# Optimization experiments

Hardware: AMD Instinct MI355X
Metric: run time of the kernel (lower is better)

The kernel has to match this reference:

```python
import jax, jax.numpy as jnp
import numpy as np

B, S, HID = 2, 2048, 2048
H, KVH, D = 16, 8, 128           # query heads, kv heads, head_dim
G = H // KVH                      # num_key_value_groups
EPS = 1e-6
SCALE = D ** -0.5
ROPE_THETA = 1e6


def _rope_tables():
    inv_freq = 1.0 / (ROPE_THETA ** (jnp.arange(0, D, 2, dtype=jnp.float32) / D))
    freqs = jnp.arange(S, dtype=jnp.float32)[:, None] * inv_freq[None, :]   # [S, D/2]
    emb = jnp.concatenate([freqs, freqs], axis=-1)                          # [S, D]
    cos = jnp.broadcast_to(jnp.cos(emb)[None], (B, S, D))
    sin = jnp.broadcast_to(jnp.sin(emb)[None], (B, S, D))
    return cos, sin


def setup_inputs() -> dict:
    key = jax.random.key(0)
    ks = jax.random.split(key, 6)
    hidden_states = jax.random.normal(ks[0], (B, S, HID), jnp.float32)
    cos, sin = _rope_tables()
    w = 0.02
    Wq = jax.random.normal(ks[1], (HID, H * D * 2), jnp.float32) * w  # gated: q + gate
    Wk = jax.random.normal(ks[2], (HID, KVH * D), jnp.float32) * w
    Wv = jax.random.normal(ks[3], (HID, KVH * D), jnp.float32) * w
    Wo = jax.random.normal(ks[4], (H * D, HID), jnp.float32) * w
    q_norm_w = jnp.ones((D,), jnp.float32)
    k_norm_w = jnp.ones((D,), jnp.float32)
    return {"hidden_states": hidden_states, "cos": cos, "sin": sin,
            "Wq": Wq, "Wk": Wk, "Wv": Wv, "Wo": Wo,
            "q_norm_w": q_norm_w, "k_norm_w": k_norm_w}


def _rms_norm(x, w):
    # per-head RMSNorm over last dim (head_dim), computed in fp32
    var = jnp.mean(jnp.square(x.astype(jnp.float32)), axis=-1, keepdims=True)
    return (x * jax.lax.rsqrt(var + EPS)) * w


def _rotate_half(x):
    x1, x2 = x[..., : D // 2], x[..., D // 2:]
    return jnp.concatenate([-x2, x1], axis=-1)


def reference(hidden_states, cos, sin, Wq, Wk, Wv, Wo, q_norm_w, k_norm_w):
    # q_proj with output gate
    mixed_q = hidden_states @ Wq                         # [B,S,H*2D]
    mixed_q = mixed_q.reshape(B, S, H, 2 * D)
    q, gate = mixed_q[..., :D], mixed_q[..., D:]          # [B,S,H,D] each
    gate = gate.reshape(B, S, H * D)
    k = (hidden_states @ Wk).reshape(B, S, KVH, D)
    v = (hidden_states @ Wv).reshape(B, S, KVH, D)

    # per-head QK RMSNorm, then to [B, heads, S, D]
    q = _rms_norm(q, q_norm_w).transpose(0, 2, 1, 3)      # [B,H,S,D]
    k = _rms_norm(k, k_norm_w).transpose(0, 2, 1, 3)      # [B,KVH,S,D]
    v = v.transpose(0, 2, 1, 3)                           # [B,KVH,S,D]

    # RoPE (cos/sin broadcast over head dim)
    c, s = cos[:, None], sin[:, None]                     # [B,1,S,D]
    q = q * c + _rotate_half(q) * s
    k = k * c + _rotate_half(k) * s

    # GQA causal attention without materializing repeated K/V
    qg = q.reshape(B, KVH, G, S, D)
    scores = jnp.einsum('bkgqd,bkld->bkgql', qg, k) * SCALE   # [B,KVH,G,S,S]
    causal = jnp.tril(jnp.ones((S, S), dtype=bool))
    scores = jnp.where(causal, scores, jnp.finfo(scores.dtype).min)
    probs = jax.nn.softmax(scores, axis=-1)
    out = jnp.einsum('bkgql,bkld->bkgqd', probs, v)           # [B,KVH,G,S,D]
    out = out.reshape(B, H, S, D).transpose(0, 2, 1, 3).reshape(B, S, H * D)

    # sigmoid-gated output, then o_proj
    out = out * jax.nn.sigmoid(gate)
    return out @ Wo
```

## Files before the change

kernel.cpp:

```cpp
#include <hip/hip_runtime.h>
#include <hip/hip_bf16.h>

#define B_ 2
#define S_ 2048
#define HID_ 2048
#define H_ 16
#define KVH_ 8
#define D_ 128
#define G_ 2
#define EPS_ 1e-6f
#define SCALE_ 0.08838834764831845f
#define SCALE2_ 0.1275313760443445f
#define NQKV 6144

typedef __hip_bfloat16 bf16;
typedef __attribute__((ext_vector_type(8))) short s8v;
typedef __attribute__((ext_vector_type(4))) float f4v;

__device__ __forceinline__ unsigned short f2b(float f) {
    __hip_bfloat16 h = __float2bfloat16(f);
    return *reinterpret_cast<unsigned short*>(&h);
}
__device__ __forceinline__ float b2f(short u) {
    unsigned int x = ((unsigned int)(unsigned short)u) << 16;
    return __builtin_bit_cast(float, x);
}

__device__ __forceinline__ f4v MFMA(s8v a, s8v b, f4v c) {
    return __builtin_amdgcn_mfma_f32_16x16x32_bf16(a, b, c, 0, 0, 0);
}

__device__ __forceinline__ void gl_lds16(const void* g, void* l) {
    __builtin_amdgcn_global_load_lds(
        (const __attribute__((address_space(1))) void*)g,
        (__attribute__((address_space(3))) void*)l, 16, 0, 0);
}

__device__ __forceinline__ void cstore(float* p, float v) { *p = v; }
__device__ __forceinline__ void cstore(short* p, float v) { *p = (short)f2b(v); }

template <int CTRL>
__device__ __forceinline__ float dpp_f(float x) {
    return __builtin_bit_cast(float,
        __builtin_amdgcn_update_dpp(0, __builtin_bit_cast(int, x), CTRL, 0xF, 0xF, true));
}
__device__ __forceinline__ float red16_max(float v) {
    v = fmaxf(v, dpp_f<0xB1>(v));
    v = fmaxf(v, dpp_f<0x4E>(v));
    v = fmaxf(v, dpp_f<0x124>(v));
    v = fmaxf(v, dpp_f<0x128>(v));
    return v;
}
__device__ __forceinline__ float red16_sum(float v) {
    v += dpp_f<0xB1>(v);
    v += dpp_f<0x4E>(v);
    v += dpp_f<0x124>(v);
    v += dpp_f<0x128>(v);
    return v;
}

__global__ __launch_bounds__(256) void f2bf_kernel(const float* __restrict__ in,
                                                   short* __restrict__ out, int n4) {
    int i = blockIdx.x * 256 + threadIdx.x;
    if (i >= n4) return;
    const float4 v = *(const float4*)(in + (size_t)i * 4);
    ushort4 o;
    o.x = f2b(v.x); o.y = f2b(v.y); o.z = f2b(v.z); o.w = f2b(v.w);
    *(ushort4*)(out + (size_t)i * 4) = o;
}

__global__ __launch_bounds__(256) void transpose_conv(const float* __restrict__ in,
                                                      short* __restrict__ out,
                                                      int K, int N) {
    __shared__ short t[32][33];
    const int n0 = blockIdx.x * 32, k0 = blockIdx.y * 32;
    const int tx = threadIdx.x, ty = threadIdx.y;
#pragma unroll
    for (int j = 0; j < 4; j++) {
        const int r = ty + j * 8;
        t[r][tx] = (short)f2b(in[(size_t)(k0 + r) * N + n0 + tx]);
    }
    __syncthreads();
#pragma unroll
    for (int j = 0; j < 4; j++) {
        const int r = ty + j * 8;
        out[(size_t)(n0 + r) * K + k0 + tx] = t[tx][r];
    }
}

__global__ __launch_bounds__(256) void transpose_v(const short* __restrict__ in,
                                                   short* __restrict__ out) {
    __shared__ short t[32][33];
    const int s0 = blockIdx.x * 32, d0 = blockIdx.y * 32, bk = blockIdx.z;
    const int b = bk / KVH_, kvh = bk % KVH_;
    const short* ip = in + (size_t)b * S_ * NQKV + kvh * D_;
    const int tx = threadIdx.x, ty = threadIdx.y;
#pragma unroll
    for (int j = 0; j < 4; j++) {
        const int r = ty + j * 8;
        t[r][tx] = ip[(size_t)(s0 + r) * NQKV + d0 + tx];
    }
    __syncthreads();
#pragma unroll
    for (int j = 0; j < 4; j++) {
        const int r = ty + j * 8;
        out[((size_t)bk * D_ + d0 + r) * S_ + s0 + tx] = t[tx][r];
    }
}

__global__ __launch_bounds__(512, 2) void gemm256(const short* __restrict__ A,
                                                  const short* __restrict__ Bt,
                                                  short* __restrict__ C,
                                                  int M, int N, int K) {
    __shared__ __align__(16) short As[3][256][32];
    __shared__ __align__(16) short Bs[3][256][32];
    const int tid = threadIdx.x;
    const int w = tid >> 6, l = tid & 63;
    const int lr = l & 15, g = l >> 4;
    const int nwg = gridDim.x * gridDim.y;
    int bid = blockIdx.y * gridDim.x + blockIdx.x;
    bid = (bid & 7) * (nwg >> 3) + (bid >> 3);
    const int bx = bid % gridDim.x, by = bid / gridDim.x;
    const int row0 = by * 256, col0 = bx * 256;
    const int wr = w >> 2, wc = w & 3;

    f4v acc[8][4];
#pragma unroll
    for (int i = 0; i < 8; i++)
#pragma unroll
        for (int j = 0; j < 4; j++) acc[i][j] = (f4v)0.f;

    const int srow = l >> 2;
    const int schunk = (l & 3) ^ ((l >> 3) & 3);
    const int rdslot = (g ^ ((lr >> 1) & 3)) * 8;

    auto stageA = [&](int buf, int t) {
        const int kt = t * 32;
#pragma unroll
        for (int i = 0; i < 2; i++) {
            const int rb = w * 32 + i * 16;
            gl_lds16(A + (size_t)(row0 + rb + srow) * K + kt + schunk * 8,
                     &As[buf][rb][0]);
        }
    };
    auto stageB = [&](int buf, int t) {
        const int kt = t * 32;
#pragma unroll
        for (int i = 0; i < 2; i++) {
            const int rb = w * 32 + i * 16;
            gl_lds16(Bt + (size_t)(col0 + rb + srow) * K + kt + schunk * 8,
                     &Bs[buf][rb][0]);
        }
    };

    const int nt = K >> 5;
    stageA(0, 0); stageB(0, 0);
    stageA(1, 1); stageB(1, 1);

#pragma unroll 1
    for (int t = 0; t < nt; t++) {
        const int buf = t % 3;
        const int nbuf = (t + 2) % 3;

        __builtin_amdgcn_sched_barrier(0);
        if (t + 1 < nt) {
            asm volatile("s_waitcnt vmcnt(4)" ::: "memory");
        } else {
            asm volatile("s_waitcnt vmcnt(0)" ::: "memory");
        }
        __builtin_amdgcn_sched_barrier(0);
        __builtin_amdgcn_s_barrier();
        __builtin_amdgcn_sched_barrier(0);

        s8v b[4], a[4];
#pragma unroll
        for (int ni = 0; ni < 4; ni++)
            b[ni] = *(const s8v*)&Bs[buf][wc * 64 + ni * 16 + lr][rdslot];
#pragma unroll
        for (int mi = 0; mi < 4; mi++)
            a[mi] = *(const s8v*)&As[buf][wr * 128 + mi * 16 + lr][rdslot];
        if (t + 2 < nt) stageA(nbuf, t + 2);
        __builtin_amdgcn_s_setprio(1);
#pragma unroll
        for (int mi = 0; mi < 4; mi++)
#pragma unroll
            for (int ni = 0; ni < 4; ni++)
                acc[mi][ni] = MFMA(a[mi], b[ni], acc[mi][ni]);
        __builtin_amdgcn_s_setprio(0);
        __builtin_amdgcn_s_barrier();
        __builtin_amdgcn_sched_barrier(0);

        s8v a2[4];
#pragma unroll
        for (int mi = 0; mi < 4; mi++)
            a2[mi] = *(const s8v*)&As[buf][wr * 128 + (4 + mi) * 16 + lr][rdslot];
        if (t + 2 < nt) stageB(nbuf, t + 2);
        __builtin_amdgcn_s_setprio(1);
#pragma unroll
        for (int mi = 0; mi < 4; mi++)
#pragma unroll
            for (int ni = 0; ni < 4; ni++)
                acc[4 + mi][ni] = MFMA(a2[mi], b[ni], acc[4 + mi][ni]);
        __builtin_amdgcn_s_setprio(0);
    }

#pragma unroll
    for (int mi = 0; mi < 8; mi++)
#pragma unroll
        for (int ni = 0; ni < 4; ni++) {
            const int row = row0 + wr * 128 + mi * 16 + g * 4;
            const int col = col0 + wc * 64 + ni * 16 + lr;
#pragma unroll
            for (int j = 0; j < 4; j++)
                cstore(&C[(size_t)(row + j) * N + col], acc[mi][ni][j]);
        }
}

template <typename CT, int GATED>
__global__ __launch_bounds__(256) void gemm_bt(const short* __restrict__ A,
                                               const short* __restrict__ Bt,
                                               CT* __restrict__ C,
                                               int M, int N, int K) {
    __shared__ __align__(16) short As[2][128][32];
    __shared__ __align__(16) short Bs[2][128][32];
    const int tid = threadIdx.x;
    const int w = tid >> 6, l = tid & 63;
    const int lr = l & 15, g = l >> 4;
    const int nwg = gridDim.x * gridDim.y;
    int bid = blockIdx.y * gridDim.x + blockIdx.x;
    bid = (bid & 7) * (nwg >> 3) + (bid >> 3);
    const int bx = bid % gridDim.x, by = bid / gridDim.x;
    const int row0 = by * 128, col0 = bx * 128;
    const int wr = w >> 1, wc = w & 1;

    f4v acc[4][4];
#pragma unroll
    for (int i = 0; i < 4; i++)
#pragma unroll
        for (int j = 0; j < 4; j++) acc[i][j] = (f4v)0.f;

    const int srow = l >> 2;
    const int sg = (l & 3) ^ ((srow >> 1) & 3);

    auto stage = [&](int buf, int kt) {
        const int k = kt + sg * 8;
#pragma unroll
        for (int i = 0; i < 2; i++) {
            const int rb = (w * 2 + i) * 16;
            size_t aoff;
            if constexpr (GATED)
                aoff = (size_t)(row0 + rb + srow) * NQKV + ((k >> 7) << 8) + (k & 127);
            else
                aoff = (size_t)(row0 + rb + srow) * K + k;
            gl_lds16(A + aoff, &As[buf][rb][0]);
            gl_lds16(Bt + (size_t)(col0 + rb + srow) * K + k, &Bs[buf][rb][0]);
        }
    };

    const int nt = K >> 5;
    stage(0, 0);
    stage(1, 32);
    const int rdslot = (g ^ ((lr >> 1) & 3)) * 8;

#pragma unroll 1
    for (int t = 0; t < nt; t++) {
        const int cur = t & 1;
        if (t + 1 < nt) {
            asm volatile("s_waitcnt vmcnt(4)" ::: "memory");
        } else {
            asm volatile("s_waitcnt vmcnt(0)" ::: "memory");
        }
        __builtin_amdgcn_s_barrier();
        __builtin_amdgcn_sched_barrier(0);

        s8v a[4], b[4];
#pragma unroll
        for (int mi = 0; mi < 4; mi++)
            a[mi] = *(const s8v*)&As[cur][wr * 64 + mi * 16 + lr][rdslot];
#pragma unroll
        for (int ni = 0; ni < 4; ni++)
            b[ni] = *(const s8v*)&Bs[cur][wc * 64 + ni * 16 + lr][rdslot];

        asm volatile("s_waitcnt lgkmcnt(0)" ::: "memory");
        __builtin_amdgcn_sched_barrier(0);
        __builtin_amdgcn_s_barrier();
        __builtin_amdgcn_sched_barrier(0);

        if (t + 2 < nt) stage(cur, (t + 2) * 32);

#pragma unroll
        for (int mi = 0; mi < 4; mi++)
#pragma unroll
            for (int ni = 0; ni < 4; ni++)
                acc[mi][ni] = MFMA(a[mi], b[ni], acc[mi][ni]);
    }

#pragma unroll
    for (int mi = 0; mi < 4; mi++)
#pragma unroll
        for (int ni = 0; ni < 4; ni++) {
            const int row = row0 + wr * 64 + mi * 16 + g * 4;
            const int col = col0 + wc * 64 + ni * 16 + lr;
#pragma unroll
            for (int j = 0; j < 4; j++)
                cstore(&C[(size_t)(row + j) * N + col], acc[mi][ni][j]);
        }
}

__global__ __launch_bounds__(128) void norm_rope(const bf16* __restrict__ src,
                                                 const float* __restrict__ normw,
                                                 const float* __restrict__ cosb,
                                                 const float* __restrict__ sinb,
                                                 bf16* __restrict__ dst,
                                                 int NH, int rowStride, int chanStride) {
    const int idx = blockIdx.x;
    const int h = idx % NH;
    const int s = (idx / NH) % S_;
    const int b = idx / (NH * S_);
    const int d = threadIdx.x;

    const size_t src_i = (size_t)(b * S_ + s) * rowStride + h * chanStride + d;
    const size_t dst_i = (((size_t)b * NH + h) * S_ + s) * D_ + d;

    float x = __bfloat162float(src[src_i]);
    float sq = x * x;
#pragma unroll
    for (int o = 32; o > 0; o >>= 1) sq += __shfl_down(sq, o);
    __shared__ float red[2];
    __shared__ float sh[128];
    if ((d & 63) == 0) red[d >> 6] = sq;
    __syncthreads();
    const float var = (red[0] + red[1]) * (1.f / 128.f);
    const float xn = x * rsqrtf(var + EPS_) * normw[d];
    sh[d] = xn;
    __syncthreads();
    const float rot = (d < 64) ? -sh[d + 64] : sh[d - 64];
    const size_t cs_i = ((size_t)b * S_ + s) * D_ + d;
    dst[dst_i] = __float2bfloat16(xn * cosb[cs_i] + rot * sinb[cs_i]);
}

__global__ __launch_bounds__(256) void flash_mfma(const short* __restrict__ qro,
                                                  const short* __restrict__ kro,
                                                  const short* __restrict__ vt,
                                                  short* __restrict__ qkv) {
    __shared__ __align__(16) short Ks[2][64][128];
    __shared__ __align__(16) short Vs[2][128][64];
    __shared__ __align__(16) short Pl[4][16][84];

    const int tid = threadIdx.x;
    const int w = tid >> 6, l = tid & 63;
    const int lr = l & 15, g = l >> 4;
    const int bx = blockIdx.x;
    const int bh = blockIdx.y;
    const int b = bh >> 4, h = bh & 15;
    const int kvh = h >> 1;

    const short* qbase = qro + (size_t)(b * H_ + h) * S_ * D_;
    const short* kbase = kro + (size_t)(b * KVH_ + kvh) * S_ * D_;
    const short* vbase = vt + (size_t)(b * KVH_ + kvh) * D_ * S_;

    auto stage = [&](int buf, int kt) {
        const int kb0 = kt * 64;
#pragma unroll
        for (int i = 0; i < 4; i++) {
            const int li = w * 4 + i;
            {
                const int r = li * 4 + (l >> 4);
                const int sgk = (l & 15) ^ (r & 7);
                gl_lds16(kbase + (size_t)(kb0 + r) * D_ + sgk * 8, &Ks[buf][li * 4][0]);
            }
            {
                const int r = li * 8 + (l >> 3);
                const int sgv = (l & 7) ^ (r & 7);
                gl_lds16(vbase + (size_t)r * S_ + kb0 + sgv * 8, &Vs[buf][li * 8][0]);
            }
        }
    };

#pragma unroll 1
    for (int seg = 0; seg < 2; seg++) {
        const int qt = seg ? bx : (31 - bx);
        const int q0 = qt * 64;
        const int qw0 = q0 + w * 16;

        if (seg) __syncthreads();

        s8v qa[4];
#pragma unroll
        for (int kc = 0; kc < 4; kc++)
            qa[kc] = *(const s8v*)(qbase + (size_t)(qw0 + lr) * D_ + kc * 32 + g * 8);

        f4v oacc[8];
#pragma unroll
        for (int i = 0; i < 8; i++) oacc[i] = (f4v)0.f;
        float m[4] = {-3e38f, -3e38f, -3e38f, -3e38f};
        float lsum[4] = {0.f, 0.f, 0.f, 0.f};

        const int nkt = qt + 1;
        stage(0, 0);
        int cur = 0;
        for (int kt = 0; kt < nkt; kt++) {
            __syncthreads();
            if (kt + 1 < nkt) stage(cur ^ 1, kt + 1);
            const int kb0 = kt * 64;

            f4v sacc[4];
#pragma unroll
            for (int ni = 0; ni < 4; ni++) sacc[ni] = (f4v)0.f;
            __builtin_amdgcn_s_setprio(1);
#pragma unroll
            for (int ni = 0; ni < 4; ni++) {
                const int r = ni * 16 + lr;
#pragma unroll
                for (int kc = 0; kc < 4; kc++) {
                    const int ph = (kc * 4 + g) ^ (r & 7);
                    const s8v kb = *(const s8v*)&Ks[cur][r][ph * 8];
                    sacc[ni] = MFMA(qa[kc], kb, sacc[ni]);
                }
            }
            __builtin_amdgcn_s_setprio(0);

            const bool masked = (kt == qt);
            float p[4][4], tmax[4];
#pragma unroll
            for (int j = 0; j < 4; j++) {
                float v0 = -3e38f;
#pragma unroll
                for (int ni = 0; ni < 4; ni++) {
                    float sc = sacc[ni][j] * SCALE2_;
                    if (masked && (kb0 + ni * 16 + lr > qw0 + g * 4 + j)) sc = -3e38f;
                    p[ni][j] = sc;
                    v0 = fmaxf(v0, sc);
                }
                tmax[j] = v0;
            }
#pragma unroll
            for (int j = 0; j < 4; j++) tmax[j] = red16_max(tmax[j]);

            bool needb = false;
#pragma unroll
            for (int j = 0; j < 4; j++) needb = needb || (tmax[j] > m[j] + 7.f);
            const bool doresc = __any((int)needb);

            float cj[4], psum[4];
#pragma unroll
            for (int j = 0; j < 4; j++) {
                float mn = m[j];
                if (doresc) {
                    mn = fmaxf(m[j], tmax[j]);
                    cj[j] = __builtin_amdgcn_exp2f(m[j] - mn);
                    m[j] = mn;
                }
                float ps = 0.f;
#pragma unroll
                for (int ni = 0; ni < 4; ni++) {
                    const float e = __builtin_amdgcn_exp2f(p[ni][j] - mn);
                    p[ni][j] = e;
                    ps += e;
                }
                psum[j] = ps;
            }

#pragma unroll
            for (int ni = 0; ni < 4; ni++)
#pragma unroll
                for (int j = 0; j < 4; j++)
                    Pl[w][g * 4 + j][ni * 16 + lr] = (short)f2b(p[ni][j]);

#pragma unroll
            for (int j = 0; j < 4; j++) psum[j] = red16_sum(psum[j]);

            if (doresc) {
#pragma unroll
                for (int j = 0; j < 4; j++) lsum[j] = lsum[j] * cj[j] + psum[j];
#pragma unroll
                for (int di = 0; di < 8; di++)
#pragma unroll
                    for (int j = 0; j < 4; j++) oacc[di][j] *= cj[j];
            } else {
#pragma unroll
                for (int j = 0; j < 4; j++) lsum[j] += psum[j];
            }

            __builtin_amdgcn_s_setprio(1);
#pragma unroll
            for (int kk = 0; kk < 2; kk++) {
                const s8v pa = *(const s8v*)&Pl[w][lr][kk * 32 + g * 8];
#pragma unroll
                for (int di = 0; di < 8; di++) {
                    const int r = di * 16 + lr;
                    const int ph = (kk * 4 + g) ^ (r & 7);
                    const s8v vb = *(const s8v*)&Vs[cur][r][ph * 8];
                    oacc[di] = MFMA(pa, vb, oacc[di]);
                }
            }
            __builtin_amdgcn_s_setprio(0);
            cur ^= 1;
        }

        float linv[4];
#pragma unroll
        for (int j = 0; j < 4; j++) linv[j] = 1.f / lsum[j];
#pragma unroll
        for (int di = 0; di < 8; di++) {
            const int d = di * 16 + lr;
#pragma unroll
            for (int j = 0; j < 4; j++) {
                const int q = qw0 + g * 4 + j;
                const size_t base = (size_t)(b * S_ + q) * NQKV + h * 256;
                const float gate = b2f(qkv[base + 128 + d]);
                const float o = oacc[di][j] * linv[j] * (1.f / (1.f + __expf(-gate)));
                qkv[base + d] = (short)f2b(o);
            }
        }
    }
}

extern "C" void kernel_launch(void* const* d_in, const int* in_sizes, int n_in,
                              void* d_out, int out_size, void* d_ws, size_t ws_size,
                              hipStream_t stream) {
    const float* hs = (const float*)d_in[0];
    const float* cosb = (const float*)d_in[1];
    const float* sinb = (const float*)d_in[2];
    const float* Wq = (const float*)d_in[3];
    const float* Wk = (const float*)d_in[4];
    const float* Wv = (const float*)d_in[5];
    const float* Wo = (const float*)d_in[6];
    const float* qnw = (const float*)d_in[7];
    const float* knw = (const float*)d_in[8];
    float* out = (float*)d_out;

    short* ws = (short*)d_ws;
    short* Wot = ws;
    short* Wt  = ws + 4194304;
    short* hsb = ws + 16777216;
    short* qkv = ws + 25165824;
    short* qro = Wt;
    short* kro = Wt + 8388608;
    short* vtb = hsb;

    const int M = B_ * S_;
    const dim3 t32x8(32, 8, 1);

    f2bf_kernel<<<8192, 256, 0, stream>>>(hs, hsb, 2097152);
    transpose_conv<<<dim3(128, 64), t32x8, 0, stream>>>(Wq, Wt, HID_, 4096);
    transpose_conv<<<dim3(32, 64), t32x8, 0, stream>>>(Wk, Wt + (size_t)4096 * 2048, HID_, 1024);
    transpose_conv<<<dim3(32, 64), t32x8, 0, stream>>>(Wv, Wt + (size_t)5120 * 2048, HID_, 1024);
    transpose_conv<<<dim3(64, 64), t32x8, 0, stream>>>(Wo, Wot, 2048, 2048);

    gemm256<<<dim3(24, 16), 512, 0, stream>>>(hsb, Wt, qkv, M, NQKV, HID_);

    norm_rope<<<dim3(B_ * S_ * H_), 128, 0, stream>>>((const bf16*)qkv, qnw, cosb, sinb,
                                                      (bf16*)qro, H_, NQKV, 256);
    norm_rope<<<dim3(B_ * S_ * KVH_), 128, 0, stream>>>((const bf16*)(qkv + 4096), knw, cosb, sinb,
                                                        (bf16*)kro, KVH_, NQKV, 128);

    transpose_v<<<dim3(64, 4, 16), t32x8, 0, stream>>>(qkv + 5120, vtb);

    flash_mfma<<<dim3(16, 32), 256, 0, stream>>>(qro, kro, vtb, qkv);

    gemm_bt<float, 1><<<dim3(16, 32), 256, 0, stream>>>(qkv, Wot, out, M, HID_, 2048);
}
```

Baseline: 326.0 us.

## Merge QKV weight transposes and norm_rope launches, retile output GEMM, fold softmax scale

Replaces the three Q/K/V weight-transpose launches with a single kernel, and merges the separate Q and K norm_rope launches into one grid. The softmax scale is folded into the stored Q values so the attention kernel no longer multiplies every score. The output projection GEMM becomes a 512-thread 256x128 tile with triple-buffered LDS, a single barrier per k-step, and MFMA priority hints. Together these aim to cut launch overhead and per-score arithmetic and to improve pipelining of the final GEMM. The trade-offs are more LDS per block and fewer blocks for the output GEMM, plus scaling Q before the bf16 conversion, which slightly changes rounding.

```diff
diff --git a/kernel.cpp b/kernel.cpp
--- a/kernel.cpp
+++ b/kernel.cpp
@@ -67,6 +67,31 @@
     ushort4 o;
     o.x = f2b(v.x); o.y = f2b(v.y); o.z = f2b(v.z); o.w = f2b(v.w);
     *(ushort4*)(out + (size_t)i * 4) = o;
+}
+
+__global__ __launch_bounds__(256) void qkvw_transpose(const float* __restrict__ Wq,
+                                                      const float* __restrict__ Wk,
+                                                      const float* __restrict__ Wv,
+                                                      short* __restrict__ out) {
+    __shared__ short t[32][33];
+    const int n0 = blockIdx.x * 32, k0 = blockIdx.y * 32;
+    const float* src;
+    int scol, sN;
+    if (n0 < 4096)      { src = Wq; scol = n0;        sN = 4096; }
+    else if (n0 < 5120) { src = Wk; scol = n0 - 4096; sN = 1024; }
+    else                { src = Wv; scol = n0 - 5120; sN = 1024; }
+    const int tx = threadIdx.x, ty = threadIdx.y;
+#pragma unroll
+    for (int j = 0; j < 4; j++) {
+        const int r = ty + j * 8;
+        t[r][tx] = (short)f2b(src[(size_t)(k0 + r) * sN + scol + tx]);
+    }
+    __syncthreads();
+#pragma unroll
+    for (int j = 0; j < 4; j++) {
+        const int r = ty + j * 8;
+        out[(size_t)(n0 + r) * HID_ + k0 + tx] = t[tx][r];
+    }
 }
 
 __global__ __launch_bounds__(256) void transpose_conv(const float* __restrict__ in,
@@ -216,13 +241,12 @@
         }
 }
 
-template <typename CT, int GATED>
-__global__ __launch_bounds__(256) void gemm_bt(const short* __restrict__ A,
-                                               const short* __restrict__ Bt,
-                                               CT* __restrict__ C,
-                                               int M, int N, int K) {
-    __shared__ __align__(16) short As[2][128][32];
-    __shared__ __align__(16) short Bs[2][128][32];
+__global__ __launch_bounds__(512, 1) void gemm_wo(const short* __restrict__ A,
+                                                  const short* __restrict__ Bt,
+                                                  float* __restrict__ C,
+                                                  int M, int N, int K) {
+    __shared__ __align__(16) short As[3][256][32];
+    __shared__ __align__(16) short Bs[3][128][32];
     const int tid = threadIdx.x;
     const int w = tid >> 6, l = tid & 63;
     const int lr = l & 15, g = l >> 4;
@@ -230,7 +254,7 @@
     int bid = blockIdx.y * gridDim.x + blockIdx.x;
     bid = (bid & 7) * (nwg >> 3) + (bid >> 3);
     const int bx = bid % gridDim.x, by = bid / gridDim.x;
-    const int row0 = by * 128, col0 = bx * 128;
+    const int row0 = by * 256, col0 = bx * 128;
     const int wr = w >> 1, wc = w & 1;
 
     f4v acc[4][4];
@@ -240,59 +264,54 @@
         for (int j = 0; j < 4; j++) acc[i][j] = (f4v)0.f;
 
     const int srow = l >> 2;
-    const int sg = (l & 3) ^ ((srow >> 1) & 3);
-
-    auto stage = [&](int buf, int kt) {
-        const int k = kt + sg * 8;
+    const int schunk = (l & 3) ^ ((l >> 3) & 3);
+    const int rdslot = (g ^ ((lr >> 1) & 3)) * 8;
+
+    auto stage = [&](int buf, int t) {
+        const int k = t * 32 + schunk * 8;
+        const size_t goff = ((size_t)((k >> 7) << 8)) + (k & 127);
 #pragma unroll
         for (int i = 0; i < 2; i++) {
-            const int rb = (w * 2 + i) * 16;
-            size_t aoff;
-            if constexpr (GATED)
-                aoff = (size_t)(row0 + rb + srow) * NQKV + ((k >> 7) << 8) + (k & 127);
-            else
-                aoff = (size_t)(row0 + rb + srow) * K + k;
-            gl_lds16(A + aoff, &As[buf][rb][0]);
-            gl_lds16(Bt + (size_t)(col0 + rb + srow) * K + k, &Bs[buf][rb][0]);
-        }
+            const int rb = w * 32 + i * 16;
+            gl_lds16(A + (size_t)(row0 + rb + srow) * NQKV + goff, &As[buf][rb][0]);
+        }
+        gl_lds16(Bt + (size_t)(col0 + w * 16 + srow) * K + k, &Bs[buf][w * 16][0]);
     };
 
     const int nt = K >> 5;
     stage(0, 0);
-    stage(1, 32);
-    const int rdslot = (g ^ ((lr >> 1) & 3)) * 8;
+    stage(1, 1);
 
 #pragma unroll 1
     for (int t = 0; t < nt; t++) {
-        const int cur = t & 1;
+        const int buf = t % 3;
+        __builtin_amdgcn_sched_barrier(0);
         if (t + 1 < nt) {
-            asm volatile("s_waitcnt vmcnt(4)" ::: "memory");
+            asm volatile("s_waitcnt vmcnt(3)" ::: "memory");
         } else {
             asm volatile("s_waitcnt vmcnt(0)" ::: "memory");
         }
+        __builtin_amdgcn_sched_barrier(0);
         __builtin_amdgcn_s_barrier();
         __builtin_amdgcn_sched_barrier(0);
 
         s8v a[4], b[4];
 #pragma unroll
         for (int mi = 0; mi < 4; mi++)
-            a[mi] = *(const s8v*)&As[cur][wr * 64 + mi * 16 + lr][rdslot];
+            a[mi] = *(const s8v*)&As[buf][wr * 64 + mi * 16 + lr][rdslot];
 #pragma unroll
         for (int ni = 0; ni < 4; ni++)
-            b[ni] = *(const s8v*)&Bs[cur][wc * 64 + ni * 16 + lr][rdslot];
-
-        asm volatile("s_waitcnt lgkmcnt(0)" ::: "memory");
-        __builtin_amdgcn_sched_barrier(0);
-        __builtin_amdgcn_s_barrier();
-        __builtin_amdgcn_sched_barrier(0);
-
-        if (t + 2 < nt) stage(cur, (t + 2) * 32);
-
+            b[ni] = *(const s8v*)&Bs[buf][wc * 64 + ni * 16 + lr][rdslot];
+
+        if (t + 2 < nt) stage((t + 2) % 3, t + 2);
+
+        __builtin_amdgcn_s_setprio(1);
 #pragma unroll
         for (int mi = 0; mi < 4; mi++)
 #pragma unroll
             for (int ni = 0; ni < 4; ni++)
                 acc[mi][ni] = MFMA(a[mi], b[ni], acc[mi][ni]);
+        __builtin_amdgcn_s_setprio(0);
     }
 
 #pragma unroll
@@ -307,22 +326,37 @@
         }
 }
 
-__global__ __launch_bounds__(128) void norm_rope(const bf16* __restrict__ src,
-                                                 const float* __restrict__ normw,
+__global__ __launch_bounds__(128) void norm_rope(const bf16* __restrict__ qkv,
+                                                 const float* __restrict__ qnw,
+                                                 const float* __restrict__ knw,
                                                  const float* __restrict__ cosb,
                                                  const float* __restrict__ sinb,
-                                                 bf16* __restrict__ dst,
-                                                 int NH, int rowStride, int chanStride) {
+                                                 bf16* __restrict__ qro,
+                                                 bf16* __restrict__ kro) {
     const int idx = blockIdx.x;
-    const int h = idx % NH;
-    const int s = (idx / NH) % S_;
-    const int b = idx / (NH * S_);
+    const int h_tot = idx % 24;
+    const int s = (idx / 24) % S_;
+    const int b = idx / (24 * S_);
     const int d = threadIdx.x;
 
-    const size_t src_i = (size_t)(b * S_ + s) * rowStride + h * chanStride + d;
-    const size_t dst_i = (((size_t)b * NH + h) * S_ + s) * D_ + d;
-
-    float x = __bfloat162float(src[src_i]);
+    const bool isQ = (h_tot < H_);
+    size_t src_i;
+    size_t dst_i;
+    const float* nw;
+    float oscale;
+    bf16* dst;
+    if (isQ) {
+        src_i = (size_t)(b * S_ + s) * NQKV + h_tot * 256 + d;
+        dst_i = (((size_t)b * H_ + h_tot) * S_ + s) * D_ + d;
+        nw = qnw; oscale = SCALE2_; dst = qro;
+    } else {
+        const int hk = h_tot - H_;
+        src_i = (size_t)(b * S_ + s) * NQKV + 4096 + hk * 128 + d;
+        dst_i = (((size_t)b * KVH_ + hk) * S_ + s) * D_ + d;
+        nw = knw; oscale = 1.f; dst = kro;
+    }
+
+    float x = __bfloat162float(qkv[src_i]);
     float sq = x * x;
 #pragma unroll
     for (int o = 32; o > 0; o >>= 1) sq += __shfl_down(sq, o);
@@ -331,12 +365,12 @@
     if ((d & 63) == 0) red[d >> 6] = sq;
     __syncthreads();
     const float var = (red[0] + red[1]) * (1.f / 128.f);
-    const float xn = x * rsqrtf(var + EPS_) * normw[d];
+    const float xn = x * rsqrtf(var + EPS_) * nw[d];
     sh[d] = xn;
     __syncthreads();
     const float rot = (d < 64) ? -sh[d + 64] : sh[d - 64];
     const size_t cs_i = ((size_t)b * S_ + s) * D_ + d;
-    dst[dst_i] = __float2bfloat16(xn * cosb[cs_i] + rot * sinb[cs_i]);
+    dst[dst_i] = __float2bfloat16((xn * cosb[cs_i] + rot * sinb[cs_i]) * oscale);
 }
 
 __global__ __launch_bounds__(256) void flash_mfma(const short* __restrict__ qro,
@@ -427,7 +461,7 @@
                 float v0 = -3e38f;
 #pragma unroll
                 for (int ni = 0; ni < 4; ni++) {
-                    float sc = sacc[ni][j] * SCALE2_;
+                    float sc = sacc[ni][j];
                     if (masked && (kb0 + ni * 16 + lr > qw0 + g * 4 + j)) sc = -3e38f;
                     p[ni][j] = sc;
                     v0 = fmaxf(v0, sc);
@@ -543,21 +577,17 @@
     const dim3 t32x8(32, 8, 1);
 
     f2bf_kernel<<<8192, 256, 0, stream>>>(hs, hsb, 2097152);
-    transpose_conv<<<dim3(128, 64), t32x8, 0, stream>>>(Wq, Wt, HID_, 4096);
-    transpose_conv<<<dim3(32, 64), t32x8, 0, stream>>>(Wk, Wt + (size_t)4096 * 2048, HID_, 1024);
-    transpose_conv<<<dim3(32, 64), t32x8, 0, stream>>>(Wv, Wt + (size_t)5120 * 2048, HID_, 1024);
+    qkvw_transpose<<<dim3(192, 64), t32x8, 0, stream>>>(Wq, Wk, Wv, Wt);
     transpose_conv<<<dim3(64, 64), t32x8, 0, stream>>>(Wo, Wot, 2048, 2048);
 
     gemm256<<<dim3(24, 16), 512, 0, stream>>>(hsb, Wt, qkv, M, NQKV, HID_);
 
-    norm_rope<<<dim3(B_ * S_ * H_), 128, 0, stream>>>((const bf16*)qkv, qnw, cosb, sinb,
-                                                      (bf16*)qro, H_, NQKV, 256);
-    norm_rope<<<dim3(B_ * S_ * KVH_), 128, 0, stream>>>((const bf16*)(qkv + 4096), knw, cosb, sinb,
-                                                        (bf16*)kro, KVH_, NQKV, 128);
+    norm_rope<<<dim3(B_ * S_ * 24), 128, 0, stream>>>((const bf16*)qkv, qnw, knw,
+                                                      cosb, sinb, (bf16*)qro, (bf16*)kro);
 
     transpose_v<<<dim3(64, 4, 16), t32x8, 0, stream>>>(qkv + 5120, vtb);
 
     flash_mfma<<<dim3(16, 32), 256, 0, stream>>>(qro, kro, vtb, qkv);
 
-    gemm_bt<float, 1><<<dim3(16, 32), 256, 0, stream>>>(qkv, Wot, out, M, HID_, 2048);
-}
+    gemm_wo<<<dim3(16, 16), 512, 0, stream>>>(qkv, Wot, out, M, HID_, 2048);
+}
```

Measured after the change: 311.6 us. 4.4% less time.
